# Kernel tuning notes

Hardware: AMD Instinct MI355X
Metric: run time of the kernel (lower is better)

Reference implementation:

```python
import jax, jax.numpy as jnp
import numpy as np

EMBED = 1024
HEADS = 16
HEAD_DIM = EMBED // HEADS
RANK = 8
ALPHA = 16
SCALE_LORA = ALPHA / RANK  # 2.0


def _lora_linear(x, W, b, A, B):
    # F.linear(x, W, b) + scale * F.linear(F.linear(x, A), B)
    return x @ W.T + b + SCALE_LORA * ((x @ A.T) @ B.T)


def setup_inputs() -> dict:
    key = jax.random.key(0)
    ks = jax.random.split(key, 17)
    d = {"x": jax.random.normal(ks[0], (2, 2048, EMBED), dtype=jnp.float32)}
    names = ["q", "k", "v", "o"]
    i = 1
    for n in names:
        d[f"W{n}"] = jax.random.normal(ks[i], (EMBED, EMBED), dtype=jnp.float32) * 0.02; i += 1
        d[f"b{n}"] = jnp.zeros((EMBED,), dtype=jnp.float32)
        d[f"A{n}"] = jax.random.normal(ks[i], (RANK, EMBED), dtype=jnp.float32) * 0.02; i += 1
        d[f"B{n}"] = jax.random.normal(ks[i], (EMBED, RANK), dtype=jnp.float32) * 0.02; i += 1
    return d


def reference(x, Wq, bq, Aq, Bq, Wk, bk, Ak, Bk, Wv, bv, Av, Bv, Wo, bo, Ao, Bo):
    N, S, _ = x.shape
    Q = _lora_linear(x, Wq, bq, Aq, Bq).reshape(N, S, HEADS, HEAD_DIM)
    K = _lora_linear(x, Wk, bk, Ak, Bk).reshape(N, S, HEADS, HEAD_DIM)
    V = _lora_linear(x, Wv, bv, Av, Bv).reshape(N, S, HEADS, HEAD_DIM)
    # energy: [N, H, Sq, Sk]
    energy = jnp.einsum("nqhd,nkhd->nhqk", Q, K) / jnp.sqrt(jnp.float32(HEAD_DIM))
    attn = jax.nn.softmax(energy, axis=-1)
    out = jnp.einsum("nhqk,nkhd->nqhd", attn, V).reshape(N, S, EMBED)
    return _lora_linear(out, Wo, bo, Ao, Bo)
```

## Files before the change

### kernel.cpp

```cpp
#include <hip/hip_runtime.h>
#include <stdint.h>

typedef uint16_t u16;
typedef short s16x8 __attribute__((ext_vector_type(8)));
typedef float f32x4 __attribute__((ext_vector_type(4)));
typedef unsigned short u16x4 __attribute__((ext_vector_type(4)));
typedef uint32_t u32;
typedef u32 u32x2 __attribute__((ext_vector_type(2)));
typedef u32 u32x4 __attribute__((ext_vector_type(4)));

#define MFMA16(a,b,c) __builtin_amdgcn_mfma_f32_16x16x32_bf16((a),(b),(c),0,0,0)
#define QSCALE 0.18033688011112042f

__device__ __forceinline__ float b2f(u16 b){
  union { u32 u; float f; } v; v.u = ((u32)b)<<16; return v.f;
}
__device__ __forceinline__ u16 f2b(float f){
  union { float f; u32 u; } v; v.f = f;
  return (u16)((v.u + 0x7fffu + ((v.u>>16)&1u))>>16);
}
__device__ __forceinline__ u32 fbits(float f){
  union { float f; u32 u; } v; v.f = f; return v.u;
}
__device__ __forceinline__ void load_lds_16B(const void* g, void* l){
  __builtin_amdgcn_global_load_lds((const __attribute__((address_space(1))) void*)g,
                                   (__attribute__((address_space(3))) void*)l, 16, 0, 0);
}

template<bool XF32, int NMAT>
__global__ __launch_bounds__(256) void lora_conv_kernel(
    const void* __restrict__ Xv,
    const float* __restrict__ A0, const float* __restrict__ A1, const float* __restrict__ A2,
    float* __restrict__ T0, float* __restrict__ T1, float* __restrict__ T2,
    u16* __restrict__ xb,
    const float* __restrict__ W0, const float* __restrict__ W1,
    const float* __restrict__ W2, const float* __restrict__ W3,
    u16* __restrict__ Wb)
{
  if (XF32 && blockIdx.x >= 1024){
    const int cv = blockIdx.x - 1024;
    const int y = cv>>8;
    const float* src = (y==0)?W0:(y==1)?W1:(y==2)?W2:W3;
    u16* dst = Wb + (size_t)y*1048576;
    const int g = (cv&255)*256 + threadIdx.x;
#pragma unroll
    for (int t=0;t<4;t++){
      const int i4 = g + t*65536;
      const f32x4 v = *(const f32x4*)(src + (size_t)i4*4);
      u16x4 o;
#pragma unroll
      for (int j=0;j<4;j++) o[j] = f2b(v[j]);
      *(u16x4*)(dst + (size_t)i4*4) = o;
    }
    return;
  }

  const int wid = threadIdx.x>>6, lane = threadIdx.x&63;
  const int m = blockIdx.x*4 + wid;

  float xf[16];
  if (XF32){
    const float* xp = (const float*)Xv + (size_t)m*1024 + lane*16;
#pragma unroll
    for (int q=0;q<4;q++){
      const f32x4 v = *(const f32x4*)(xp + q*4);
#pragma unroll
      for (int j=0;j<4;j++) xf[q*4+j] = v[j];
    }
    u16* xbp = xb + (size_t)m*1024 + lane*16;
#pragma unroll
    for (int q=0;q<4;q++){
      u16x4 o;
#pragma unroll
      for (int j=0;j<4;j++) o[j] = f2b(xf[q*4+j]);
      *(u16x4*)(xbp + q*4) = o;
    }
  } else {
    const u16* xp = (const u16*)Xv + (size_t)m*1024 + lane*16;
#pragma unroll
    for (int j=0;j<16;j++) xf[j] = b2f(xp[j]);
  }

#pragma unroll
  for (int mat=0; mat<NMAT; mat++){
    const float* A = (mat==0)?A0:(mat==1)?A1:A2;
    float* T = (mat==0)?T0:(mat==1)?T1:T2;
    float accv[8];
#pragma unroll
    for (int r=0;r<8;r++){
      const float* ap = A + r*1024 + lane*16;
      float s = 0.f;
#pragma unroll
      for (int q=0;q<4;q++){
        const f32x4 av = *(const f32x4*)(ap + q*4);
#pragma unroll
        for (int j=0;j<4;j++) s += xf[q*4+j]*av[j];
      }
      accv[r] = s;
    }
#pragma unroll
    for (int r=0;r<8;r++){
      float s = accv[r];
      s += __shfl_xor(s,1);  s += __shfl_xor(s,2);  s += __shfl_xor(s,4);
      s += __shfl_xor(s,8);  s += __shfl_xor(s,16); s += __shfl_xor(s,32);
      accv[r] = s;
    }
    if (lane==0){
#pragma unroll
      for (int r=0;r<8;r++) T[(size_t)m*8 + r] = accv[r];
    }
  }
}

__global__ __launch_bounds__(256,2) void gemm_qkv_kernel(
    const u16* __restrict__ Xb, const u16* __restrict__ Wb,
    const float* __restrict__ bq, const float* __restrict__ bk, const float* __restrict__ bv,
    const float* __restrict__ tq, const float* __restrict__ tk, const float* __restrict__ tv,
    const float* __restrict__ Blq, const float* __restrict__ Blk, const float* __restrict__ Blv,
    u16* __restrict__ Qb, u16* __restrict__ Kb, u16* __restrict__ Vtb)
{
  __shared__ u16 sm[16896];
  u16* AtB = sm;
  u16* BtB = sm + 8192;
  const int tid = threadIdx.x;
  const int wid = tid>>6, lane = tid&63;
  const int quad = lane>>4, l16 = lane&15;
  const int wm = wid>>1, wn = wid&1;
  const int proj = blockIdx.x>>3;
  const int n0 = (blockIdx.x&7)<<7, m0 = blockIdx.y<<7;
  const u16* W = Wb + (size_t)proj*1048576;
  const float* bias = (proj==0)?bq:(proj==1)?bk:bv;
  const float* T    = (proj==0)?tq:(proj==1)?tk:tv;
  const float* Bl   = (proj==0)?Blq:(proj==1)?Blk:Blv;
  const float scale = (proj==0)?QSCALE:1.0f;

  f32x4 acc[4][4];
#pragma unroll
  for (int i=0;i<4;i++)
#pragma unroll
    for (int j=0;j<4;j++) acc[i][j] = f32x4{0.f,0.f,0.f,0.f};

  for (int k0=0;k0<1024;k0+=64){
#pragma unroll
    for (int half=0; half<2; half++){
#pragma unroll
      for (int p=0;p<2;p++){
        const int s = wid*128 + p*64 + lane;
        const int row = s>>2, c = s&3;
        load_lds_16B(Xb + (size_t)(m0+row)*1024 + k0 + half*32 + c*8, AtB + half*4096 + (wid*128+p*64)*8);
        load_lds_16B(W  + (size_t)(n0+row)*1024 + k0 + half*32 + c*8, BtB + half*4096 + (wid*128+p*64)*8);
      }
    }
    __syncthreads();
#pragma unroll
    for (int half=0; half<2; half++){
      s16x8 af[4], bfr[4];
#pragma unroll
      for (int t=0;t<4;t++){
        const int r = wm*64 + t*16 + l16;
        af[t]  = *(const s16x8*)(AtB + half*4096 + r*32 + quad*8);
        const int c = wn*64 + t*16 + l16;
        bfr[t] = *(const s16x8*)(BtB + half*4096 + c*32 + quad*8);
      }
#pragma unroll
      for (int tm=0;tm<4;tm++)
#pragma unroll
        for (int tn=0;tn<4;tn++)
          acc[tm][tn] = MFMA16(af[tm], bfr[tn], acc[tm][tn]);
    }
    __syncthreads();
  }

  s16x8 tf[4], bfl[4];
#pragma unroll
  for (int t=0;t<4;t++){ tf[t] = s16x8{0,0,0,0,0,0,0,0}; bfl[t] = s16x8{0,0,0,0,0,0,0,0}; }
  if (quad==0){
#pragma unroll
    for (int tm=0;tm<4;tm++){
      const float* tp = T + (size_t)(m0 + wm*64 + tm*16 + l16)*8;
      const f32x4 a0 = *(const f32x4*)(tp);
      const f32x4 a1 = *(const f32x4*)(tp+4);
#pragma unroll
      for (int j=0;j<4;j++){ tf[tm][j] = (short)f2b(2.0f*a0[j]); tf[tm][4+j] = (short)f2b(2.0f*a1[j]); }
    }
#pragma unroll
    for (int tn=0;tn<4;tn++){
      const float* bp = Bl + (size_t)(n0 + wn*64 + tn*16 + l16)*8;
      const f32x4 b0 = *(const f32x4*)(bp);
      const f32x4 b1 = *(const f32x4*)(bp+4);
#pragma unroll
      for (int j=0;j<4;j++){ bfl[tn][j] = (short)f2b(b0[j]); bfl[tn][4+j] = (short)f2b(b1[j]); }
    }
  }
#pragma unroll
  for (int tm=0;tm<4;tm++)
#pragma unroll
    for (int tn=0;tn<4;tn++)
      acc[tm][tn] = MFMA16(tf[tm], bfl[tn], acc[tm][tn]);

  if (proj==2){
#pragma unroll
    for (int tn=0;tn<4;tn++){
      const int nl = wn*64 + tn*16 + l16;
      const float bn = bias[n0+nl];
#pragma unroll
      for (int tm=0;tm<4;tm++){
        const int ml = wm*64 + tm*16 + quad*4;
        u16x4 pk;
#pragma unroll
        for (int rg=0;rg<4;rg++) pk[rg] = f2b(acc[tm][tn][rg]+bn);
        *(u16x4*)(sm + nl*132 + ml) = pk;
      }
    }
    __syncthreads();
    const int batch = m0>>11, sbase = m0&2047;
#pragma unroll
    for (int p=0;p<8;p++){
      const int idx = p*256 + tid;
      const int row = idx>>4, c16 = idx&15;
      const s16x8 v = *(const s16x8*)(sm + row*132 + c16*8);
      const int ng = n0 + row, hh = ng>>6, dd = ng&63;
      *(s16x8*)(Vtb + (size_t)((batch*16+hh)*64+dd)*2048 + sbase + c16*8) = v;
    }
  } else {
#pragma unroll
    for (int tn=0;tn<4;tn++){
      const int n = n0 + wn*64 + tn*16 + l16;
      const float bn = bias[n];
#pragma unroll
      for (int tm=0;tm<4;tm++){
        const int mb = m0 + wm*64 + tm*16 + quad*4;
        if (proj==0){
#pragma unroll
          for (int rg=0;rg<4;rg++) Qb[(size_t)(mb+rg)*1024 + n] = f2b((acc[tm][tn][rg]+bn)*scale);
        } else {
#pragma unroll
          for (int rg=0;rg<4;rg++) Kb[(size_t)(mb+rg)*1024 + n] = f2b(acc[tm][tn][rg]+bn);
        }
      }
    }
  }
}

__global__ __launch_bounds__(256,2) void gemm_o_kernel(
    const u16* __restrict__ Xb, const u16* __restrict__ W,
    const float* __restrict__ bias, const float* __restrict__ T,
    const float* __restrict__ Bl, float* __restrict__ Out)
{
  __shared__ u16 At[2][128*32];
  __shared__ u16 Bt[2][64*32];
  const int tid = threadIdx.x;
  const int wid = tid>>6, lane = tid&63;
  const int quad = lane>>4, l16 = lane&15;
  const int wm = wid>>1, wn = wid&1;
  const int m0 = blockIdx.y<<7, n0 = blockIdx.x<<6;

  f32x4 acc[4][2];
#pragma unroll
  for (int i=0;i<4;i++)
#pragma unroll
    for (int j=0;j<2;j++) acc[i][j] = f32x4{0.f,0.f,0.f,0.f};

  for (int k0=0;k0<1024;k0+=64){
#pragma unroll
    for (int half=0; half<2; half++){
#pragma unroll
      for (int p=0;p<2;p++){
        const int s = wid*128 + p*64 + lane;
        const int row = s>>2, c = s&3;
        load_lds_16B(Xb + (size_t)(m0+row)*1024 + k0 + half*32 + c*8, At[half] + (wid*128+p*64)*8);
      }
      { const int s = wid*64 + lane;
        const int row = s>>2, c = s&3;
        load_lds_16B(W + (size_t)(n0+row)*1024 + k0 + half*32 + c*8, Bt[half] + (wid*64)*8); }
    }
    __syncthreads();
#pragma unroll
    for (int half=0; half<2; half++){
      s16x8 af[4], bfr[2];
#pragma unroll
      for (int t=0;t<4;t++){
        const int r = wm*64 + t*16 + l16;
        af[t] = *(const s16x8*)(At[half] + r*32 + quad*8);
      }
#pragma unroll
      for (int t=0;t<2;t++){
        const int c = wn*32 + t*16 + l16;
        bfr[t] = *(const s16x8*)(Bt[half] + c*32 + quad*8);
      }
#pragma unroll
      for (int tm=0;tm<4;tm++)
#pragma unroll
        for (int tn=0;tn<2;tn++)
          acc[tm][tn] = MFMA16(af[tm], bfr[tn], acc[tm][tn]);
    }
    __syncthreads();
  }

  s16x8 tf[4], bfl[2];
#pragma unroll
  for (int t=0;t<4;t++) tf[t] = s16x8{0,0,0,0,0,0,0,0};
#pragma unroll
  for (int t=0;t<2;t++) bfl[t] = s16x8{0,0,0,0,0,0,0,0};
  if (quad==0){
#pragma unroll
    for (int tm=0;tm<4;tm++){
      const float* tp = T + (size_t)(m0 + wm*64 + tm*16 + l16)*8;
      const f32x4 a0 = *(const f32x4*)(tp);
      const f32x4 a1 = *(const f32x4*)(tp+4);
#pragma unroll
      for (int j=0;j<4;j++){ tf[tm][j] = (short)f2b(2.0f*a0[j]); tf[tm][4+j] = (short)f2b(2.0f*a1[j]); }
    }
#pragma unroll
    for (int tn=0;tn<2;tn++){
      const float* bp = Bl + (size_t)(n0 + wn*32 + tn*16 + l16)*8;
      const f32x4 b0 = *(const f32x4*)(bp);
      const f32x4 b1 = *(const f32x4*)(bp+4);
#pragma unroll
      for (int j=0;j<4;j++){ bfl[tn][j] = (short)f2b(b0[j]); bfl[tn][4+j] = (short)f2b(b1[j]); }
    }
  }
#pragma unroll
  for (int tm=0;tm<4;tm++)
#pragma unroll
    for (int tn=0;tn<2;tn++)
      acc[tm][tn] = MFMA16(tf[tm], bfl[tn], acc[tm][tn]);

#pragma unroll
  for (int tn=0;tn<2;tn++){
    const int n = n0 + wn*32 + tn*16 + l16;
    const float bn = bias[n];
#pragma unroll
    for (int tm=0;tm<4;tm++){
      const int mb = m0 + wm*64 + tm*16 + quad*4;
#pragma unroll
      for (int rg=0;rg<4;rg++)
        Out[(size_t)(mb+rg)*1024 + n] = acc[tm][tn][rg] + bn;
    }
  }
}

__global__ __launch_bounds__(512,4) void attn_kernel(
    const u16* __restrict__ Q, const u16* __restrict__ K,
    const u16* __restrict__ Vt, u16* __restrict__ Out)
{
  __shared__ u16 KtB[2][128*72];
  __shared__ u16 VtB[2][64*136];
  const int tid = threadIdx.x;
  const int wid = tid>>6, lane = tid&63;
  const int quad = lane>>4, l16 = lane&15;
  const int lin = blockIdx.x + (blockIdx.y<<4) + (blockIdx.z<<8);
  const int swz = (lin&7)*64 + (lin>>3);
  const int q0 = (swz&15)<<7;
  const int h  = (swz>>4)&15;
  const int nb = swz>>8;
  const int qg = wid>>1;
  const int kh = wid&1;
  const int qw = qg*32;

  s16x8 qf[2][2];
#pragma unroll
  for (int g=0;g<2;g++){
    const int row = q0 + qw + g*16 + l16;
#pragma unroll
    for (int dh=0;dh<2;dh++)
      qf[g][dh] = *(const s16x8*)(Q + (size_t)(nb*2048+row)*1024 + h*64 + dh*32 + quad*8);
  }
  f32x4 OT[2][4];
  f32x4 Lacc[2];
#pragma unroll
  for (int g=0;g<2;g++){
#pragma unroll
    for (int td=0;td<4;td++) OT[g][td] = f32x4{0.f,0.f,0.f,0.f};
    Lacc[g] = f32x4{0.f,0.f,0.f,0.f};
  }
  s16x8 ones;
#pragma unroll
  for (int j=0;j<8;j++) ones[j] = (short)0x3F80;

  s16x8 kreg[2], vreg[2];
  auto LOADT = [&](int kn){
#pragma unroll
    for (int p=0;p<2;p++){
      const int s = p*512 + tid;
      kreg[p] = *(const s16x8*)(K + (size_t)(nb*2048+kn+(s>>3))*1024 + h*64 + (s&7)*8);
      vreg[p] = *(const s16x8*)(Vt + (size_t)((nb*16+h)*64+(s>>4))*2048 + kn + (s&15)*8);
    }
  };
  auto WRITET = [&](int b){
    u16* Ktb = KtB[b]; u16* Vtb = VtB[b];
#pragma unroll
    for (int p=0;p<2;p++){
      const int s = p*512 + tid;
      *(s16x8*)(Ktb + (s>>3)*72 + (s&7)*8) = kreg[p];
      *(s16x8*)(Vtb + (s>>4)*136 + (s&15)*8) = vreg[p];
    }
  };

  LOADT(0);
  WRITET(0);
  LOADT(128);
  __syncthreads();

  for (int t=0;t<16;t++){
    const int cur = t&1;
    if (t < 15) WRITET(cur^1);
    if (t < 14) LOADT((t+2)*128);
    const u16* KtC = KtB[cur];
    const u16* VtC = VtB[cur];

#pragma unroll
    for (int kb=0;kb<2;kb++){
      u32 ew[2][2], ow[2][2];
#pragma unroll
      for (int sel=0;sel<2;sel++){
        const int key = kh*64 + kb*32 + sel*16 + l16;
        const s16x8 kf0 = *(const s16x8*)(KtC + key*72 + quad*8);
        const s16x8 kf1 = *(const s16x8*)(KtC + key*72 + 32 + quad*8);
#pragma unroll
        for (int g=0;g<2;g++){
          f32x4 z = f32x4{0.f,0.f,0.f,0.f};
          z = MFMA16(kf0, qf[g][0], z);
          z = MFMA16(kf1, qf[g][1], z);
          const float p0 = __builtin_amdgcn_exp2f(z[0]);
          const float p1 = __builtin_amdgcn_exp2f(z[1]);
          const float p2 = __builtin_amdgcn_exp2f(z[2]);
          const float p3 = __builtin_amdgcn_exp2f(z[3]);
          const u32 w0 = __builtin_amdgcn_perm(fbits(p1), fbits(p0), 0x07060302u);
          const u32 w1 = __builtin_amdgcn_perm(fbits(p3), fbits(p2), 0x07060302u);
          if (sel==0){ ew[g][0]=w0; ew[g][1]=w1; } else { ow[g][0]=w0; ow[g][1]=w1; }
        }
      }
      s16x8 pf[2];
#pragma unroll
      for (int g=0;g<2;g++){
        const u32x2 r32 = __builtin_amdgcn_permlane32_swap(ew[g][0], ow[g][0], false, false);
        const u32x2 r16 = __builtin_amdgcn_permlane16_swap(r32[0], r32[1], false, false);
        const u32x2 s32 = __builtin_amdgcn_permlane32_swap(ew[g][1], ow[g][1], false, false);
        const u32x2 s16v = __builtin_amdgcn_permlane16_swap(s32[0], s32[1], false, false);
        u32x4 pw; pw[0]=r16[0]; pw[1]=s16v[0]; pw[2]=r16[1]; pw[3]=s16v[1];
        pf[g] = __builtin_bit_cast(s16x8, pw);
      }
      __builtin_amdgcn_s_setprio(1);
#pragma unroll
      for (int td=0;td<4;td++){
        const s16x8 vf = *(const s16x8*)(VtC + (td*16+l16)*136 + kh*64 + kb*32 + quad*8);
#pragma unroll
        for (int g=0;g<2;g++)
          OT[g][td] = MFMA16(vf, pf[g], OT[g][td]);
      }
#pragma unroll
      for (int g=0;g<2;g++)
        Lacc[g] = MFMA16(ones, pf[g], Lacc[g]);
      __builtin_amdgcn_s_setprio(0);
    }
    __syncthreads();
  }

  float* ep = (float*)KtB;
  float* lw = (float*)VtB;
  if (kh==1){
#pragma unroll
    for (int g=0;g<2;g++){
      const int q = qw + g*16 + l16;
#pragma unroll
      for (int td=0;td<4;td++)
        *(f32x4*)(ep + q*68 + td*16 + quad*4) = OT[g][td];
      if (quad==0) lw[q] = Lacc[g][0];
    }
  }
  __syncthreads();
  if (kh==0){
#pragma unroll
    for (int g=0;g<2;g++){
      const int q = qw + g*16 + l16;
      const float linv = 1.0f / (Lacc[g][0] + lw[q]);
      const int qout = q0 + q;
#pragma unroll
      for (int td=0;td<4;td++){
        const f32x4 o2 = *(const f32x4*)(ep + q*68 + td*16 + quad*4);
        u16x4 pk;
#pragma unroll
        for (int rg=0;rg<4;rg++) pk[rg] = f2b((OT[g][td][rg]+o2[rg])*linv);
        *(u16x4*)(Out + (size_t)(nb*2048+qout)*1024 + h*64 + td*16 + quad*4) = pk;
      }
    }
  }
}

extern "C" void kernel_launch(void* const* d_in, const int* in_sizes, int n_in,
                              void* d_out, int out_size, void* d_ws, size_t ws_size,
                              hipStream_t stream)
{
  const float* x  = (const float*)d_in[0];
  const float* Wq = (const float*)d_in[1];  const float* bq = (const float*)d_in[2];
  const float* Aq = (const float*)d_in[3];  const float* Bq = (const float*)d_in[4];
  const float* Wk = (const float*)d_in[5];  const float* bk = (const float*)d_in[6];
  const float* Ak = (const float*)d_in[7];  const float* Bk = (const float*)d_in[8];
  const float* Wv = (const float*)d_in[9];  const float* bv = (const float*)d_in[10];
  const float* Av = (const float*)d_in[11]; const float* Bv = (const float*)d_in[12];
  const float* Wo = (const float*)d_in[13]; const float* bo = (const float*)d_in[14];
  const float* Ao = (const float*)d_in[15]; const float* Bo = (const float*)d_in[16];

  char* ws = (char*)d_ws;
  float* tq = (float*)(ws + 0);
  float* tk = (float*)(ws + 131072);
  float* tv = (float*)(ws + 262144);
  float* to = (float*)(ws + 393216);
  u16* xb  = (u16*)(ws + 524288);
  u16* Ab  = xb;
  u16* Wb  = (u16*)(ws + 524288 + 8388608);
  u16* Qb  = (u16*)(ws + 524288 + 2*8388608);
  u16* Kb  = (u16*)(ws + 524288 + 3*8388608);
  u16* Vtb = (u16*)(ws + 524288 + 4*8388608);

  lora_conv_kernel<true,3><<<dim3(2048),256,0,stream>>>(
      x, Aq, Ak, Av, tq, tk, tv, xb, Wq, Wk, Wv, Wo, Wb);
  gemm_qkv_kernel<<<dim3(24,32),256,0,stream>>>(xb, Wb, bq, bk, bv, tq, tk, tv,
                                                Bq, Bk, Bv, Qb, Kb, Vtb);
  attn_kernel<<<dim3(16,16,2),512,0,stream>>>(Qb, Kb, Vtb, Ab);
  lora_conv_kernel<false,1><<<dim3(1024),256,0,stream>>>(
      Ab, Ao, Ao, Ao, to, to, to, nullptr,
      nullptr, nullptr, nullptr, nullptr, nullptr);
  gemm_o_kernel<<<dim3(16,32),256,0,stream>>>(Ab, Wb + (size_t)3*1048576, bo, to, Bo,
                                              (float*)d_out);
}
```

Baseline: 229.1 us.

## Fuse LoRA down-projection into GEMM main loops via extra MFMA

Removes the separate fp32 LoRA down-projection kernels (x@A^T) for the QKV and output projections. A is converted once to bf16, zero-padded to 16 rows, and each GEMM accumulates x@A^T with one extra MFMA per tile step, reusing the A-operand fragments already in registers. The result is staged through shared memory to build the rank-8 up-projection operand. This drops one kernel launch and a full extra read of the activations, but adds MFMA work, an extra global load per k-step and an extra barrier, and now computes the down-projection in bf16 instead of fp32.

```diff
diff --git a/kernel.cpp b/kernel.cpp
--- a/kernel.cpp
+++ b/kernel.cpp
@@ -27,18 +27,31 @@
                                    (__attribute__((address_space(3))) void*)l, 16, 0, 0);
 }
 
-template<bool XF32, int NMAT>
-__global__ __launch_bounds__(256) void lora_conv_kernel(
-    const void* __restrict__ Xv,
-    const float* __restrict__ A0, const float* __restrict__ A1, const float* __restrict__ A2,
-    float* __restrict__ T0, float* __restrict__ T1, float* __restrict__ T2,
-    u16* __restrict__ xb,
+__global__ __launch_bounds__(256) void conv_kernel(
+    const float* __restrict__ x, u16* __restrict__ xb,
     const float* __restrict__ W0, const float* __restrict__ W1,
     const float* __restrict__ W2, const float* __restrict__ W3,
-    u16* __restrict__ Wb)
+    u16* __restrict__ Wb,
+    const float* __restrict__ A0, const float* __restrict__ A1,
+    const float* __restrict__ A2, const float* __restrict__ A3,
+    u16* __restrict__ Abf)
 {
-  if (XF32 && blockIdx.x >= 1024){
-    const int cv = blockIdx.x - 1024;
+  const int bid = blockIdx.x;
+  if (bid < 1024){
+    const int g = bid*256 + threadIdx.x;
+#pragma unroll
+    for (int t=0;t<4;t++){
+      const int i4 = g + t*262144;
+      const f32x4 v = *(const f32x4*)(x + (size_t)i4*4);
+      u16x4 o;
+#pragma unroll
+      for (int j=0;j<4;j++) o[j] = f2b(v[j]);
+      *(u16x4*)(xb + (size_t)i4*4) = o;
+    }
+    return;
+  }
+  if (bid < 2048){
+    const int cv = bid - 1024;
     const int y = cv>>8;
     const float* src = (y==0)?W0:(y==1)?W1:(y==2)?W2:W3;
     u16* dst = Wb + (size_t)y*1048576;
@@ -54,68 +67,27 @@
     }
     return;
   }
-
-  const int wid = threadIdx.x>>6, lane = threadIdx.x&63;
-  const int m = blockIdx.x*4 + wid;
-
-  float xf[16];
-  if (XF32){
-    const float* xp = (const float*)Xv + (size_t)m*1024 + lane*16;
-#pragma unroll
-    for (int q=0;q<4;q++){
-      const f32x4 v = *(const f32x4*)(xp + q*4);
-#pragma unroll
-      for (int j=0;j<4;j++) xf[q*4+j] = v[j];
-    }
-    u16* xbp = xb + (size_t)m*1024 + lane*16;
-#pragma unroll
-    for (int q=0;q<4;q++){
-      u16x4 o;
-#pragma unroll
-      for (int j=0;j<4;j++) o[j] = f2b(xf[q*4+j]);
-      *(u16x4*)(xbp + q*4) = o;
-    }
-  } else {
-    const u16* xp = (const u16*)Xv + (size_t)m*1024 + lane*16;
-#pragma unroll
-    for (int j=0;j<16;j++) xf[j] = b2f(xp[j]);
-  }
-
-#pragma unroll
-  for (int mat=0; mat<NMAT; mat++){
-    const float* A = (mat==0)?A0:(mat==1)?A1:A2;
-    float* T = (mat==0)?T0:(mat==1)?T1:T2;
-    float accv[8];
-#pragma unroll
-    for (int r=0;r<8;r++){
-      const float* ap = A + r*1024 + lane*16;
-      float s = 0.f;
-#pragma unroll
-      for (int q=0;q<4;q++){
-        const f32x4 av = *(const f32x4*)(ap + q*4);
-#pragma unroll
-        for (int j=0;j<4;j++) s += xf[q*4+j]*av[j];
-      }
-      accv[r] = s;
-    }
-#pragma unroll
-    for (int r=0;r<8;r++){
-      float s = accv[r];
-      s += __shfl_xor(s,1);  s += __shfl_xor(s,2);  s += __shfl_xor(s,4);
-      s += __shfl_xor(s,8);  s += __shfl_xor(s,16); s += __shfl_xor(s,32);
-      accv[r] = s;
-    }
-    if (lane==0){
-#pragma unroll
-      for (int r=0;r<8;r++) T[(size_t)m*8 + r] = accv[r];
-    }
+  for (int w = threadIdx.x; w < 8192; w += 256){
+    const int proj = w >> 11, rem = w & 2047;
+    const int row = rem >> 7, c8 = (rem & 127) << 3;
+    u16x4 o0 = u16x4{0,0,0,0}, o1 = u16x4{0,0,0,0};
+    if (row < 8){
+      const float* ap = ((proj==0)?A0:(proj==1)?A1:(proj==2)?A2:A3) + row*1024 + c8;
+      const f32x4 v0 = *(const f32x4*)(ap);
+      const f32x4 v1 = *(const f32x4*)(ap+4);
+#pragma unroll
+      for (int j=0;j<4;j++){ o0[j] = f2b(v0[j]); o1[j] = f2b(v1[j]); }
+    }
+    u16* dp = Abf + (size_t)(proj*16 + row)*1024 + c8;
+    *(u16x4*)(dp)   = o0;
+    *(u16x4*)(dp+4) = o1;
   }
 }
 
 __global__ __launch_bounds__(256,2) void gemm_qkv_kernel(
     const u16* __restrict__ Xb, const u16* __restrict__ Wb,
     const float* __restrict__ bq, const float* __restrict__ bk, const float* __restrict__ bv,
-    const float* __restrict__ tq, const float* __restrict__ tk, const float* __restrict__ tv,
+    const u16* __restrict__ Abf,
     const float* __restrict__ Blq, const float* __restrict__ Blk, const float* __restrict__ Blv,
     u16* __restrict__ Qb, u16* __restrict__ Kb, u16* __restrict__ Vtb)
 {
@@ -129,16 +101,19 @@
   const int proj = blockIdx.x>>3;
   const int n0 = (blockIdx.x&7)<<7, m0 = blockIdx.y<<7;
   const u16* W = Wb + (size_t)proj*1048576;
+  const u16* AbP = Abf + (size_t)proj*16384;
   const float* bias = (proj==0)?bq:(proj==1)?bk:bv;
-  const float* T    = (proj==0)?tq:(proj==1)?tk:tv;
   const float* Bl   = (proj==0)?Blq:(proj==1)?Blk:Blv;
   const float scale = (proj==0)?QSCALE:1.0f;
 
   f32x4 acc[4][4];
-#pragma unroll
-  for (int i=0;i<4;i++)
+  f32x4 acc_t[4];
+#pragma unroll
+  for (int i=0;i<4;i++){
 #pragma unroll
     for (int j=0;j<4;j++) acc[i][j] = f32x4{0.f,0.f,0.f,0.f};
+    acc_t[i] = f32x4{0.f,0.f,0.f,0.f};
+  }
 
   for (int k0=0;k0<1024;k0+=64){
 #pragma unroll
@@ -162,14 +137,27 @@
         const int c = wn*64 + t*16 + l16;
         bfr[t] = *(const s16x8*)(BtB + half*4096 + c*32 + quad*8);
       }
-#pragma unroll
-      for (int tm=0;tm<4;tm++)
+      const s16x8 abf = *(const s16x8*)(AbP + (size_t)l16*1024 + k0 + half*32 + quad*8);
+#pragma unroll
+      for (int tm=0;tm<4;tm++){
 #pragma unroll
         for (int tn=0;tn<4;tn++)
           acc[tm][tn] = MFMA16(af[tm], bfr[tn], acc[tm][tn]);
-    }
-    __syncthreads();
-  }
+        acc_t[tm] = MFMA16(af[tm], abf, acc_t[tm]);
+      }
+    }
+    __syncthreads();
+  }
+
+  float* tT = (float*)sm;
+  if (wn==0 && l16<8){
+#pragma unroll
+    for (int tm=0;tm<4;tm++)
+#pragma unroll
+      for (int rg=0;rg<4;rg++)
+        tT[(wm*64 + tm*16 + quad*4 + rg)*8 + l16] = acc_t[tm][rg];
+  }
+  __syncthreads();
 
   s16x8 tf[4], bfl[4];
 #pragma unroll
@@ -177,11 +165,9 @@
   if (quad==0){
 #pragma unroll
     for (int tm=0;tm<4;tm++){
-      const float* tp = T + (size_t)(m0 + wm*64 + tm*16 + l16)*8;
-      const f32x4 a0 = *(const f32x4*)(tp);
-      const f32x4 a1 = *(const f32x4*)(tp+4);
-#pragma unroll
-      for (int j=0;j<4;j++){ tf[tm][j] = (short)f2b(2.0f*a0[j]); tf[tm][4+j] = (short)f2b(2.0f*a1[j]); }
+      const float* tp = tT + (wm*64 + tm*16 + l16)*8;
+#pragma unroll
+      for (int j=0;j<8;j++) tf[tm][j] = (short)f2b(2.0f*tp[j]);
     }
 #pragma unroll
     for (int tn=0;tn<4;tn++){
@@ -199,6 +185,7 @@
       acc[tm][tn] = MFMA16(tf[tm], bfl[tn], acc[tm][tn]);
 
   if (proj==2){
+    __syncthreads();
 #pragma unroll
     for (int tn=0;tn<4;tn++){
       const int nl = wn*64 + tn*16 + l16;
@@ -244,7 +231,7 @@
 
 __global__ __launch_bounds__(256,2) void gemm_o_kernel(
     const u16* __restrict__ Xb, const u16* __restrict__ W,
-    const float* __restrict__ bias, const float* __restrict__ T,
+    const float* __restrict__ bias, const u16* __restrict__ Abf,
     const float* __restrict__ Bl, float* __restrict__ Out)
 {
   __shared__ u16 At[2][128*32];
@@ -254,12 +241,16 @@
   const int quad = lane>>4, l16 = lane&15;
   const int wm = wid>>1, wn = wid&1;
   const int m0 = blockIdx.y<<7, n0 = blockIdx.x<<6;
+  const u16* AbP = Abf + (size_t)3*16384;
 
   f32x4 acc[4][2];
-#pragma unroll
-  for (int i=0;i<4;i++)
+  f32x4 acc_t[4];
+#pragma unroll
+  for (int i=0;i<4;i++){
 #pragma unroll
     for (int j=0;j<2;j++) acc[i][j] = f32x4{0.f,0.f,0.f,0.f};
+    acc_t[i] = f32x4{0.f,0.f,0.f,0.f};
+  }
 
   for (int k0=0;k0<1024;k0+=64){
 #pragma unroll
@@ -288,14 +279,27 @@
         const int c = wn*32 + t*16 + l16;
         bfr[t] = *(const s16x8*)(Bt[half] + c*32 + quad*8);
       }
-#pragma unroll
-      for (int tm=0;tm<4;tm++)
+      const s16x8 abf = *(const s16x8*)(AbP + (size_t)l16*1024 + k0 + half*32 + quad*8);
+#pragma unroll
+      for (int tm=0;tm<4;tm++){
 #pragma unroll
         for (int tn=0;tn<2;tn++)
           acc[tm][tn] = MFMA16(af[tm], bfr[tn], acc[tm][tn]);
-    }
-    __syncthreads();
-  }
+        acc_t[tm] = MFMA16(af[tm], abf, acc_t[tm]);
+      }
+    }
+    __syncthreads();
+  }
+
+  float* tT = (float*)At;
+  if (wn==0 && l16<8){
+#pragma unroll
+    for (int tm=0;tm<4;tm++)
+#pragma unroll
+      for (int rg=0;rg<4;rg++)
+        tT[(wm*64 + tm*16 + quad*4 + rg)*8 + l16] = acc_t[tm][rg];
+  }
+  __syncthreads();
 
   s16x8 tf[4], bfl[2];
 #pragma unroll
@@ -305,11 +309,9 @@
   if (quad==0){
 #pragma unroll
     for (int tm=0;tm<4;tm++){
-      const float* tp = T + (size_t)(m0 + wm*64 + tm*16 + l16)*8;
-      const f32x4 a0 = *(const f32x4*)(tp);
-      const f32x4 a1 = *(const f32x4*)(tp+4);
-#pragma unroll
-      for (int j=0;j<4;j++){ tf[tm][j] = (short)f2b(2.0f*a0[j]); tf[tm][4+j] = (short)f2b(2.0f*a1[j]); }
+      const float* tp = tT + (wm*64 + tm*16 + l16)*8;
+#pragma unroll
+      for (int j=0;j<8;j++) tf[tm][j] = (short)f2b(2.0f*tp[j]);
     }
 #pragma unroll
     for (int tn=0;tn<2;tn++){
@@ -503,10 +505,7 @@
   const float* Ao = (const float*)d_in[15]; const float* Bo = (const float*)d_in[16];
 
   char* ws = (char*)d_ws;
-  float* tq = (float*)(ws + 0);
-  float* tk = (float*)(ws + 131072);
-  float* tv = (float*)(ws + 262144);
-  float* to = (float*)(ws + 393216);
+  u16* Abf = (u16*)(ws + 0);
   u16* xb  = (u16*)(ws + 524288);
   u16* Ab  = xb;
   u16* Wb  = (u16*)(ws + 524288 + 8388608);
@@ -514,14 +513,11 @@
   u16* Kb  = (u16*)(ws + 524288 + 3*8388608);
   u16* Vtb = (u16*)(ws + 524288 + 4*8388608);
 
-  lora_conv_kernel<true,3><<<dim3(2048),256,0,stream>>>(
-      x, Aq, Ak, Av, tq, tk, tv, xb, Wq, Wk, Wv, Wo, Wb);
-  gemm_qkv_kernel<<<dim3(24,32),256,0,stream>>>(xb, Wb, bq, bk, bv, tq, tk, tv,
+  conv_kernel<<<dim3(2049),256,0,stream>>>(x, xb, Wq, Wk, Wv, Wo, Wb,
+                                           Aq, Ak, Av, Ao, Abf);
+  gemm_qkv_kernel<<<dim3(24,32),256,0,stream>>>(xb, Wb, bq, bk, bv, Abf,
                                                 Bq, Bk, Bv, Qb, Kb, Vtb);
   attn_kernel<<<dim3(16,16,2),512,0,stream>>>(Qb, Kb, Vtb, Ab);
-  lora_conv_kernel<false,1><<<dim3(1024),256,0,stream>>>(
-      Ab, Ao, Ao, Ao, to, to, to, nullptr,
-      nullptr, nullptr, nullptr, nullptr, nullptr);
-  gemm_o_kernel<<<dim3(16,32),256,0,stream>>>(Ab, Wb + (size_t)3*1048576, bo, to, Bo,
+  gemm_o_kernel<<<dim3(16,32),256,0,stream>>>(Ab, Wb + (size_t)3*1048576, bo, Abf, Bo,
                                               (float*)d_out);
 }
```

After: 220.9 us (median of 3 runs). 3.6% less time.
